# Performance work log

Hardware: AMD Instinct MI355X
Metric: run time of the kernel (lower is better)

## Reference

```python
import jax, jax.numpy as jnp
import numpy as np

N, C_IN, C_OUT = 8192, 256, 128
NEG_SLOPE = 0.2


def setup_inputs() -> dict:
    key = jax.random.key(0)
    k0, k1, k2, k3, k4 = jax.random.split(key, 5)
    x = jax.random.normal(k0, (N, C_IN), dtype=jnp.float32)
    # sparse-ish binary dense adjacency, avg degree ~32
    adj = (jax.random.uniform(k1, (N, N)) < (32.0 / N)).astype(jnp.float32)
    W = jax.random.normal(k2, (C_IN, C_OUT), dtype=jnp.float32) * 0.05
    att_src = jax.random.normal(k3, (C_OUT,), dtype=jnp.float32) * 0.1
    att_dst = jax.random.normal(k4, (C_OUT,), dtype=jnp.float32) * 0.1
    bias = jnp.zeros((C_OUT,), dtype=jnp.float32)
    return {"x": x, "adj": adj, "W": W, "att_src": att_src,
            "att_dst": att_dst, "bias": bias}


def reference(x, adj, W, att_src, att_dst, bias):
    n = adj.shape[0]
    idx = jnp.arange(n)
    adj = adj.at[idx, idx].set(1.0)          # add self loops
    h = x @ W                                 # [N, C_out]
    a_src = h @ att_src                       # [N]
    a_dst = h @ att_dst                       # [N]
    alpha = a_src[:, None] + a_dst[None, :]   # [N, N]
    alpha = jax.nn.leaky_relu(alpha, NEG_SLOPE)
    alpha = adj * jnp.exp(alpha)              # masked exp
    alpha = alpha / alpha.sum(axis=0, keepdims=True)  # column-normalize (dim=0)
    out = (adj * alpha).T @ h + bias          # [N, C_out]
    return out
```

## Files before the change

kernel.cpp:

```cpp
#include <hip/hip_runtime.h>
#include <hip/hip_bf16.h>

#define NN 8192
#define CIN 256
#define COUT 128
#define GR 16
#define GKT 64
#define CH 8
#define ICH (NN / CH)
#define KT 64

typedef unsigned short u16;
typedef _Float16 f16;
typedef __attribute__((ext_vector_type(8))) short short8;
typedef __attribute__((ext_vector_type(8))) _Float16 f16x8;
typedef __attribute__((ext_vector_type(16))) float f32x16;

__device__ __forceinline__ short8 pack8_bf16(const float* v) {
    union { __hip_bfloat162 b2[4]; short8 s; } u;
    #pragma unroll
    for (int q = 0; q < 4; ++q)
        u.b2[q] = __float22bfloat162_rn(make_float2(v[2 * q], v[2 * q + 1]));
    return u.s;
}

__device__ __forceinline__ void load_lds16(const float* g, float* l) {
    __builtin_amdgcn_global_load_lds(
        (const __attribute__((address_space(1))) void*)g,
        (__attribute__((address_space(3))) void*)l, 16, 0, 0);
}

__global__ __launch_bounds__(256) void gemm_h(const float* __restrict__ x,
                                              const float* __restrict__ W,
                                              const float* __restrict__ att_src,
                                              const float* __restrict__ att_dst,
                                              u16* __restrict__ h_t,
                                              float* __restrict__ a_src,
                                              float* __restrict__ a_dst) {
    __shared__ float Wt[GKT * COUT];
    __shared__ float xt[GKT][GR + 2];
    __shared__ float ot[GR][COUT + 4];
    int tid = threadIdx.x;
    int i0 = blockIdx.x * GR;
    int tx = tid & 31, ty = tid >> 5;
    int c0 = tx * 4, r0 = ty * 2;
    int xr = tid >> 4, xk = (tid & 15) * 4;
    float acc[2][4] = {};

    for (int kt = 0; kt < CIN; kt += GKT) {
        float4 wv[8];
        #pragma unroll
        for (int j = 0; j < 8; ++j) {
            int f = j * 256 + tid;
            wv[j] = *(const float4*)&W[(size_t)(kt + (f >> 5)) * COUT + (f & 31) * 4];
        }
        float4 xv = *(const float4*)&x[(size_t)(i0 + xr) * CIN + kt + xk];
        __syncthreads();
        #pragma unroll
        for (int j = 0; j < 8; ++j)
            *(float4*)&Wt[(j * 256 + tid) * 4] = wv[j];
        xt[xk + 0][xr] = xv.x;
        xt[xk + 1][xr] = xv.y;
        xt[xk + 2][xr] = xv.z;
        xt[xk + 3][xr] = xv.w;
        __syncthreads();
        #pragma unroll 8
        for (int k = 0; k < GKT; ++k) {
            float4 wk = *(const float4*)&Wt[k * COUT + c0];
            float2 xf = *(const float2*)&xt[k][r0];
            acc[0][0] += xf.x * wk.x; acc[0][1] += xf.x * wk.y;
            acc[0][2] += xf.x * wk.z; acc[0][3] += xf.x * wk.w;
            acc[1][0] += xf.y * wk.x; acc[1][1] += xf.y * wk.y;
            acc[1][2] += xf.y * wk.z; acc[1][3] += xf.y * wk.w;
        }
    }

    float4 asv = *(const float4*)&att_src[c0];
    float4 adv = *(const float4*)&att_dst[c0];
    #pragma unroll
    for (int a = 0; a < 2; ++a) {
        float4 o = make_float4(acc[a][0], acc[a][1], acc[a][2], acc[a][3]);
        *(float4*)&ot[r0 + a][c0] = o;
        float s = o.x * asv.x + o.y * asv.y + o.z * asv.z + o.w * asv.w;
        float d = o.x * adv.x + o.y * adv.y + o.z * adv.z + o.w * adv.w;
        #pragma unroll
        for (int m = 16; m >= 1; m >>= 1) {
            s += __shfl_xor(s, m, 32);
            d += __shfl_xor(d, m, 32);
        }
        if (tx == 0) {
            a_src[i0 + r0 + a] = s;
            a_dst[i0 + r0 + a] = d;
        }
    }
    __syncthreads();
    int c = tid >> 1, hf = tid & 1;
    float vals[8];
    #pragma unroll
    for (int q = 0; q < 8; ++q) vals[q] = ot[hf * 8 + q][c];
    short8 pk = pack8_bf16(vals);
    *(short8*)(h_t + (size_t)c * NN + i0 + hf * 8) = pk;
}

__global__ __launch_bounds__(256) void gat_mm(const float* __restrict__ adj,
                                              const u16* __restrict__ h_t,
                                              const float* __restrict__ a_src,
                                              const float* __restrict__ a_dst,
                                              f16* __restrict__ pout,
                                              float* __restrict__ pden) {
    __shared__ float tileA[KT * COUT];
    __shared__ float asrcS[ICH];
    int tid = threadIdx.x;
    int lane = tid & 63, w = tid >> 6;
    int jb = blockIdx.x & 63, ch = blockIdx.x >> 6;
    int j0 = jb * 128;
    int i0 = ch * ICH;
    int half = lane >> 5;
    int jloc = w * 32 + (lane & 31);
    int gj = j0 + jloc;
    float dj = a_dst[gj];

    ((float4*)asrcS)[tid] = ((const float4*)(a_src + i0))[tid];

    f32x16 acc[4];
    #pragma unroll
    for (int nt = 0; nt < 4; ++nt)
        #pragma unroll
        for (int q = 0; q < 16; ++q) acc[nt][q] = 0.f;
    float dsum = 0.f;
    __syncthreads();

    for (int s = 0; s < ICH / KT; ++s) {
        int ib = i0 + s * KT;
        #pragma unroll
        for (int q = 0; q < 8; ++q) {
            int f = q * 256 + tid;
            const float* gp = adj + (size_t)(ib + (f >> 5)) * NN + j0 + (f & 31) * 4;
            load_lds16(gp, &tileA[f * 4]);
        }
        __syncthreads();
        #pragma unroll
        for (int kk = 0; kk < 4; ++kk) {
            int kb = kk * 16 + half * 8;
            int gib = ib + kb;
            short8 bf[4];
            #pragma unroll
            for (int nt = 0; nt < 4; ++nt) {
                int c = nt * 32 + (lane & 31);
                bf[nt] = *(const short8*)(h_t + (size_t)c * NN + gib);
            }
            float av[8];
            #pragma unroll
            for (int e = 0; e < 8; ++e)
                av[e] = tileA[(kb + e) * COUT + jloc];
            float4 s0 = *(const float4*)&asrcS[s * KT + kb];
            float4 s1 = *(const float4*)&asrcS[s * KT + kb + 4];
            float sv[8] = {s0.x, s0.y, s0.z, s0.w, s1.x, s1.y, s1.z, s1.w};
            float pv[8];
            #pragma unroll
            for (int e = 0; e < 8; ++e) {
                float t = sv[e] + dj;
                float ev = __expf(fmaxf(t, 0.2f * t));
                int gi = gib + e;
                pv[e] = (av[e] != 0.f || gi == gj) ? ev : 0.f;
                dsum += pv[e];
            }
            short8 af = pack8_bf16(pv);
            #pragma unroll
            for (int nt = 0; nt < 4; ++nt)
                acc[nt] = __builtin_amdgcn_mfma_f32_32x32x16_bf16(af, bf[nt],
                                                                  acc[nt], 0, 0, 0);
        }
        __syncthreads();
    }

    #pragma unroll
    for (int nt = 0; nt < 4; ++nt) {
        int c = nt * 32 + (lane & 31);
        #pragma unroll
        for (int r = 0; r < 16; ++r) {
            int row = (r & 3) + 8 * (r >> 2) + 4 * half;
            int j = j0 + w * 32 + row;
            pout[((size_t)ch * NN + j) * COUT + c] = (f16)acc[nt][r];
        }
    }
    float dall = dsum + __shfl_xor(dsum, 32, 64);
    if (half == 0) pden[(size_t)ch * NN + gj] = dall;
}

__global__ __launch_bounds__(256) void gat_reduce(const f16* __restrict__ pout,
                                                  const float* __restrict__ pden,
                                                  const float* __restrict__ bias,
                                                  float* __restrict__ out) {
    int idx = blockIdx.x * 256 + threadIdx.x;
    int j = idx >> 4;
    int c8 = (idx & 15) * 8;
    f16x8 pv[CH];
    #pragma unroll
    for (int ch = 0; ch < CH; ++ch)
        pv[ch] = *(const f16x8*)(pout + ((size_t)ch * NN + j) * COUT + c8);
    float den = 0.f;
    #pragma unroll
    for (int ch = 0; ch < CH; ++ch) den += pden[(size_t)ch * NN + j];
    float s[8] = {};
    #pragma unroll
    for (int ch = 0; ch < CH; ++ch)
        #pragma unroll
        for (int q = 0; q < 8; ++q) s[q] += (float)pv[ch][q];
    float inv = 1.0f / den;
    float4 b0 = *(const float4*)&bias[c8];
    float4 b1 = *(const float4*)&bias[c8 + 4];
    float4 o0 = make_float4(s[0] * inv + b0.x, s[1] * inv + b0.y,
                            s[2] * inv + b0.z, s[3] * inv + b0.w);
    float4 o1 = make_float4(s[4] * inv + b1.x, s[5] * inv + b1.y,
                            s[6] * inv + b1.z, s[7] * inv + b1.w);
    *(float4*)&out[(size_t)j * COUT + c8]     = o0;
    *(float4*)&out[(size_t)j * COUT + c8 + 4] = o1;
}

extern "C" void kernel_launch(void* const* d_in, const int* in_sizes, int n_in,
                              void* d_out, int out_size, void* d_ws, size_t ws_size,
                              hipStream_t stream) {
    const float* x       = (const float*)d_in[0];
    const float* adj     = (const float*)d_in[1];
    const float* W       = (const float*)d_in[2];
    const float* att_src = (const float*)d_in[3];
    const float* att_dst = (const float*)d_in[4];
    const float* bias    = (const float*)d_in[5];
    float* out = (float*)d_out;

    u16*   h_t   = (u16*)d_ws;
    float* a_src = (float*)((char*)d_ws + (size_t)2 * 1024 * 1024);
    float* a_dst = a_src + NN;
    float* pden  = a_dst + NN;
    f16*   pout  = (f16*)(pden + (size_t)CH * NN);

    gemm_h    <<<NN / GR, 256, 0, stream>>>(x, W, att_src, att_dst, h_t, a_src, a_dst);
    gat_mm    <<<64 * CH, 256, 0, stream>>>(adj, h_t, a_src, a_dst, pout, pden);
    gat_reduce<<<NN * COUT / 8 / 256, 256, 0, stream>>>(pout, pden, bias, out);
}
```

Baseline: 420.6 us.

## Stage h_t tiles in LDS for gat_mm and enlarge gemm_h row tile

In gat_mm, each K-step now loads the 128x64 bf16 slice of h_t cooperatively into a padded LDS buffer, and the MFMA B-operands are read from LDS. Previously each wave read them straight from global memory, so all four waves fetched the same data separately. Separately, gemm_h now computes 32 rows per block instead of 16, with each thread holding a 4x4 accumulator, which improves reuse of the W tile and halves the block count. The cost is extra LDS (about 18KB more per block), which may lower occupancy, plus register-held staging loads before the barrier.

```diff
diff --git a/kernel.cpp b/kernel.cpp
--- a/kernel.cpp
+++ b/kernel.cpp
@@ -4,11 +4,12 @@
 #define NN 8192
 #define CIN 256
 #define COUT 128
-#define GR 16
+#define GR 32
 #define GKT 64
 #define CH 8
 #define ICH (NN / CH)
 #define KT 64
+#define HTS 72
 
 typedef unsigned short u16;
 typedef _Float16 f16;
@@ -38,14 +39,14 @@
                                               float* __restrict__ a_src,
                                               float* __restrict__ a_dst) {
     __shared__ float Wt[GKT * COUT];
-    __shared__ float xt[GKT][GR + 2];
+    __shared__ float xt[GKT][GR + 4];
     __shared__ float ot[GR][COUT + 4];
     int tid = threadIdx.x;
     int i0 = blockIdx.x * GR;
     int tx = tid & 31, ty = tid >> 5;
-    int c0 = tx * 4, r0 = ty * 2;
-    int xr = tid >> 4, xk = (tid & 15) * 4;
-    float acc[2][4] = {};
+    int c0 = tx * 4, r0 = ty * 4;
+    int xr = tid >> 3, xk = (tid & 7) * 8;
+    float acc[4][4] = {};
 
     for (int kt = 0; kt < CIN; kt += GKT) {
         float4 wv[8];
@@ -54,31 +55,34 @@
             int f = j * 256 + tid;
             wv[j] = *(const float4*)&W[(size_t)(kt + (f >> 5)) * COUT + (f & 31) * 4];
         }
-        float4 xv = *(const float4*)&x[(size_t)(i0 + xr) * CIN + kt + xk];
+        float4 xv0 = *(const float4*)&x[(size_t)(i0 + xr) * CIN + kt + xk];
+        float4 xv1 = *(const float4*)&x[(size_t)(i0 + xr) * CIN + kt + xk + 4];
         __syncthreads();
         #pragma unroll
         for (int j = 0; j < 8; ++j)
             *(float4*)&Wt[(j * 256 + tid) * 4] = wv[j];
-        xt[xk + 0][xr] = xv.x;
-        xt[xk + 1][xr] = xv.y;
-        xt[xk + 2][xr] = xv.z;
-        xt[xk + 3][xr] = xv.w;
+        xt[xk + 0][xr] = xv0.x; xt[xk + 1][xr] = xv0.y;
+        xt[xk + 2][xr] = xv0.z; xt[xk + 3][xr] = xv0.w;
+        xt[xk + 4][xr] = xv1.x; xt[xk + 5][xr] = xv1.y;
+        xt[xk + 6][xr] = xv1.z; xt[xk + 7][xr] = xv1.w;
         __syncthreads();
         #pragma unroll 8
         for (int k = 0; k < GKT; ++k) {
             float4 wk = *(const float4*)&Wt[k * COUT + c0];
-            float2 xf = *(const float2*)&xt[k][r0];
-            acc[0][0] += xf.x * wk.x; acc[0][1] += xf.x * wk.y;
-            acc[0][2] += xf.x * wk.z; acc[0][3] += xf.x * wk.w;
-            acc[1][0] += xf.y * wk.x; acc[1][1] += xf.y * wk.y;
-            acc[1][2] += xf.y * wk.z; acc[1][3] += xf.y * wk.w;
+            float4 xf = *(const float4*)&xt[k][r0];
+            float xa[4] = {xf.x, xf.y, xf.z, xf.w};
+            #pragma unroll
+            for (int a = 0; a < 4; ++a) {
+                acc[a][0] += xa[a] * wk.x; acc[a][1] += xa[a] * wk.y;
+                acc[a][2] += xa[a] * wk.z; acc[a][3] += xa[a] * wk.w;
+            }
         }
     }
 
     float4 asv = *(const float4*)&att_src[c0];
     float4 adv = *(const float4*)&att_dst[c0];
     #pragma unroll
-    for (int a = 0; a < 2; ++a) {
+    for (int a = 0; a < 4; ++a) {
         float4 o = make_float4(acc[a][0], acc[a][1], acc[a][2], acc[a][3]);
         *(float4*)&ot[r0 + a][c0] = o;
         float s = o.x * asv.x + o.y * asv.y + o.z * asv.z + o.w * asv.w;
@@ -95,11 +99,11 @@
     }
     __syncthreads();
     int c = tid >> 1, hf = tid & 1;
-    float vals[8];
-    #pragma unroll
-    for (int q = 0; q < 8; ++q) vals[q] = ot[hf * 8 + q][c];
-    short8 pk = pack8_bf16(vals);
-    *(short8*)(h_t + (size_t)c * NN + i0 + hf * 8) = pk;
+    float vals[16];
+    #pragma unroll
+    for (int q = 0; q < 16; ++q) vals[q] = ot[hf * 16 + q][c];
+    *(short8*)(h_t + (size_t)c * NN + i0 + hf * 16)     = pack8_bf16(vals);
+    *(short8*)(h_t + (size_t)c * NN + i0 + hf * 16 + 8) = pack8_bf16(vals + 8);
 }
 
 __global__ __launch_bounds__(256) void gat_mm(const float* __restrict__ adj,
@@ -109,6 +113,7 @@
                                               f16* __restrict__ pout,
                                               float* __restrict__ pden) {
     __shared__ float tileA[KT * COUT];
+    __shared__ u16 htS[128 * HTS];
     __shared__ float asrcS[ICH];
     int tid = threadIdx.x;
     int lane = tid & 63, w = tid >> 6;
@@ -138,7 +143,19 @@
             const float* gp = adj + (size_t)(ib + (f >> 5)) * NN + j0 + (f & 31) * 4;
             load_lds16(gp, &tileA[f * 4]);
         }
-        __syncthreads();
+        short8 bv[4];
+        int bc[4], bi[4];
+        #pragma unroll
+        for (int q = 0; q < 4; ++q) {
+            int p = q * 256 + tid;
+            bc[q] = p >> 3; bi[q] = (p & 7) * 8;
+            bv[q] = *(const short8*)(h_t + (size_t)bc[q] * NN + ib + bi[q]);
+        }
+        #pragma unroll
+        for (int q = 0; q < 4; ++q)
+            *(short8*)(htS + bc[q] * HTS + bi[q]) = bv[q];
+        __syncthreads();
+
         #pragma unroll
         for (int kk = 0; kk < 4; ++kk) {
             int kb = kk * 16 + half * 8;
@@ -147,7 +164,7 @@
             #pragma unroll
             for (int nt = 0; nt < 4; ++nt) {
                 int c = nt * 32 + (lane & 31);
-                bf[nt] = *(const short8*)(h_t + (size_t)c * NN + gib);
+                bf[nt] = *(const short8*)(htS + c * HTS + kb);
             }
             float av[8];
             #pragma unroll
```

Measured after the change: 398.2 us. -5.3%, faster.
